# Performance work log

Hardware: AMD Instinct MI355X
Metric: run time of the kernel (lower is better)

The kernel has to match this reference:

```python
import jax, jax.numpy as jnp
import numpy as np

G = 8
NEIGHBORS = 9
EPS = 1e-5


def grid_sample_bilinear_border(img, grid):
    # img: [B, C, H, W], grid: [B, Hg, Wg, 2] with (x, y) in [-1, 1]
    # matches torch.nn.functional.grid_sample(mode='bilinear', padding_mode='border', align_corners=False)
    B, C, H, W = img.shape
    gx, gy = grid[..., 0], grid[..., 1]
    ix = jnp.clip(((gx + 1.0) * W - 1.0) * 0.5, 0.0, W - 1.0)
    iy = jnp.clip(((gy + 1.0) * H - 1.0) * 0.5, 0.0, H - 1.0)
    x0 = jnp.floor(ix); y0 = jnp.floor(iy)
    x1 = x0 + 1.0;      y1 = y0 + 1.0
    w00 = (x1 - ix) * (y1 - iy)
    w01 = (ix - x0) * (y1 - iy)
    w10 = (x1 - ix) * (iy - y0)
    w11 = (ix - x0) * (iy - y0)
    x0i = jnp.clip(x0, 0, W - 1).astype(jnp.int32)
    x1i = jnp.clip(x1, 0, W - 1).astype(jnp.int32)
    y0i = jnp.clip(y0, 0, H - 1).astype(jnp.int32)
    y1i = jnp.clip(y1, 0, H - 1).astype(jnp.int32)

    def gather(im, yy, xx):  # im [C,H,W], yy/xx [Hg,Wg] -> [C,Hg,Wg]
        return im[:, yy, xx]

    g = jax.vmap(gather)
    out = (g(img, y0i, x0i) * w00[:, None]
         + g(img, y0i, x1i) * w01[:, None]
         + g(img, y1i, x0i) * w10[:, None]
         + g(img, y1i, x1i) * w11[:, None])
    return out  # [B, C, Hg, Wg]


def pconv(x, w):
    # 1x1x1 conv3d (no bias): x [B,Cin,D,H,W], w [Cout,Cin]
    return jnp.einsum('bcdhw,oc->bodhw', x, w)


def bn_relu(x, gamma, beta):
    # BatchNorm3d (training-mode batch stats, biased variance) + ReLU
    mean = jnp.mean(x, axis=(0, 2, 3, 4), keepdims=True)
    var = jnp.var(x, axis=(0, 2, 3, 4), keepdims=True)
    xn = (x - mean) * jax.lax.rsqrt(var + EPS)
    return jax.nn.relu(xn * gamma.reshape(1, -1, 1, 1, 1) + beta.reshape(1, -1, 1, 1, 1))


def setup_inputs() -> dict:
    key = jax.random.key(0)
    ks = jax.random.split(key, 8)
    B, C, H, W = 2, 64, 256, 320
    ref_feature = jax.random.normal(ks[0], (B, C, H, W), dtype=jnp.float32)
    grid = jax.random.uniform(ks[1], (B, NEIGHBORS * H, W, 2), dtype=jnp.float32,
                              minval=-1.0, maxval=1.0)
    s0 = 1.0 / np.sqrt(G)
    w0 = jax.random.uniform(ks[2], (16, G), jnp.float32, -s0, s0)
    g0 = jnp.ones((16,), jnp.float32); b0 = jnp.zeros((16,), jnp.float32)
    s1 = 1.0 / np.sqrt(16)
    w1 = jax.random.uniform(ks[3], (8, 16), jnp.float32, -s1, s1)
    g1 = jnp.ones((8,), jnp.float32); b1 = jnp.zeros((8,), jnp.float32)
    s2 = 1.0 / np.sqrt(8)
    ws = jax.random.uniform(ks[4], (1, 8), jnp.float32, -s2, s2)
    bs = jax.random.uniform(ks[5], (1,), jnp.float32, -s2, s2)
    return {"ref_feature": ref_feature, "grid": grid,
            "w0": w0, "g0": g0, "b0": b0,
            "w1": w1, "g1": g1, "b1": b1,
            "ws": ws, "bs": bs}


def reference(ref_feature, grid, w0, g0, b0, w1, g1, b1, ws, bs):
    B, C, H, W = ref_feature.shape
    x = grid_sample_bilinear_border(ref_feature, grid)          # [B, C, 9H, W]
    ref = ref_feature.reshape(B, G, C // G, H, W)               # [B, G, C/G, H, W]
    x = x.reshape(B, G, C // G, NEIGHBORS, H, W)
    x = jnp.mean(x * ref[:, :, :, None], axis=2)                # [B, G, 9, H, W]
    x = bn_relu(pconv(x, w0), g0, b0)                           # [B, 16, 9, H, W]
    x = bn_relu(pconv(x, w1), g1, b1)                           # [B, 8, 9, H, W]
    s = pconv(x, ws) + bs.reshape(1, -1, 1, 1, 1)               # [B, 1, 9, H, W]
    return jax.nn.sigmoid(jnp.squeeze(s, axis=1))               # [B, 9, H, W]
```

## Files before the change

kernel.cpp:

```cpp
#include <hip/hip_runtime.h>
#include <math.h>


constexpr int   Bc  = 2;
constexpr int   Cc  = 64;
constexpr int   Hc  = 256;
constexpr int   Wc  = 320;
constexpr int   NBc = 9;
constexpr int   HWc = Hc * Wc;
constexpr int   NPIX = Bc * HWc;
constexpr int   NPT  = Bc * NBc * HWc;
constexpr float EPSV = 1e-5f;

constexpr int NBLK_S = NPIX / 32;
constexpr int NB1    = 1024;
constexpr int NB2    = 1024;

constexpr size_t OFF_FEATB = 0;
constexpr size_t OFF_SB    = OFF_FEATB + (size_t)NPIX * 32;
constexpr size_t OFF_YM    = OFF_SB + (size_t)NPT * 4;
constexpr size_t OFF_ZM    = OFF_YM + 32;

__device__ __forceinline__ unsigned short f2bf_rne(float v) {
  unsigned int u = __float_as_uint(v);
  unsigned int r = (u + 0x7fffu + ((u >> 16) & 1u)) >> 16;
  return (unsigned short)r;
}
__device__ __forceinline__ void unpack8(uint4 u, float f[8]) {
  f[0] = __uint_as_float(u.x << 16);
  f[1] = __uint_as_float(u.x & 0xffff0000u);
  f[2] = __uint_as_float(u.y << 16);
  f[3] = __uint_as_float(u.y & 0xffff0000u);
  f[4] = __uint_as_float(u.z << 16);
  f[5] = __uint_as_float(u.z & 0xffff0000u);
  f[6] = __uint_as_float(u.w << 16);
  f[7] = __uint_as_float(u.w & 0xffff0000u);
}

__global__ __launch_bounds__(256) void k_transpose(
    const float* __restrict__ feat, unsigned short* __restrict__ featB,
    float* __restrict__ ymom) {
  if (blockIdx.x == 0 && threadIdx.x < 48) ymom[threadIdx.x] = 0.f;
  __shared__ float lds[64][65];
  const int tid  = threadIdx.x;
  const int b    = blockIdx.x / (HWc / 64);
  const int tile = blockIdx.x % (HWc / 64);
  const int hw0  = tile * 64;
  const int p    = tid & 63;
  const int ty   = tid >> 6;

  const float* src = feat + (size_t)b * Cc * HWc + hw0 + p;
#pragma unroll
  for (int c0 = 0; c0 < 64; c0 += 4) {
    lds[c0 + ty][p] = src[(size_t)(c0 + ty) * HWc];
  }
  __syncthreads();
  const int ch = tid & 63;
  unsigned short* dst = featB + ((size_t)b * HWc + hw0) * 64 + ch;
#pragma unroll
  for (int p0 = 0; p0 < 64; p0 += 4) {
    dst[(size_t)(p0 + ty) * 64] = f2bf_rne(lds[ch][p0 + ty]);
  }
}

__global__ __launch_bounds__(256) void k_sample(
    const float* __restrict__ grid, const unsigned short* __restrict__ featB,
    unsigned short* __restrict__ sOut) {
  const int tid = threadIdx.x;
  const int cid = blockIdx.x * 32 + (tid >> 3);
  const int j   = tid & 7;
  const int b   = cid / HWc;
  const int hw  = cid - b * HWc;
  const int h   = hw / Wc;
  const int w   = hw - h * Wc;

  const uint4* fbAll = (const uint4*)featB;
  const uint4 ur = fbAll[(size_t)cid * 8 + j];
  float r[8];
  unpack8(ur, r);

  const uint4* fb = fbAll + (size_t)b * HWc * 8;

#pragma unroll 3
  for (int n = 0; n < NBc; ++n) {
    const size_t gi = ((((size_t)b * NBc + n) * Hc + h) * Wc + w) * 2;
    const float2 g2 = *(const float2*)(grid + gi);
    float ix = ((g2.x + 1.f) * (float)Wc - 1.f) * 0.5f;
    float iy = ((g2.y + 1.f) * (float)Hc - 1.f) * 0.5f;
    ix = fminf(fmaxf(ix, 0.f), (float)(Wc - 1));
    iy = fminf(fmaxf(iy, 0.f), (float)(Hc - 1));
    const float x0f = floorf(ix), y0f = floorf(iy);
    const float fx = ix - x0f, fy = iy - y0f;
    const int x0 = (int)x0f, y0 = (int)y0f;
    const int x1 = min(x0 + 1, Wc - 1), y1 = min(y0 + 1, Hc - 1);
    const float w00 = (1.f - fx) * (1.f - fy);
    const float w01 = fx * (1.f - fy);
    const float w10 = (1.f - fx) * fy;
    const float w11 = fx * fy;

    const uint4 u00 = fb[(size_t)(y0 * Wc + x0) * 8 + j];
    const uint4 u01 = fb[(size_t)(y0 * Wc + x1) * 8 + j];
    const uint4 u10 = fb[(size_t)(y1 * Wc + x0) * 8 + j];
    const uint4 u11 = fb[(size_t)(y1 * Wc + x1) * 8 + j];
    float a[8], c[8], d[8], e[8];
    unpack8(u00, a);
    unpack8(u01, c);
    unpack8(u10, d);
    unpack8(u11, e);

    float s = 0.f;
#pragma unroll
    for (int k = 0; k < 8; ++k) {
      s += (w00 * a[k] + w01 * c[k] + w10 * d[k] + w11 * e[k]) * r[k];
    }
    s *= 0.125f;

    const size_t pt = ((size_t)b * NBc + n) * HWc + hw;
    sOut[pt * 8 + j] = f2bf_rne(s);
  }
}

__global__ __launch_bounds__(256) void k_stats1(
    const unsigned short* __restrict__ sB, const float* __restrict__ w0,
    float* __restrict__ ymom) {
  __shared__ float w0s[128];
  __shared__ float red[4 * 32];
  const int tid = threadIdx.x;
  if (tid < 128) w0s[tid] = w0[tid];
  __syncthreads();

  float sy[16], sy2[16];
#pragma unroll
  for (int c = 0; c < 16; ++c) { sy[c] = 0.f; sy2[c] = 0.f; }

  const int stride = gridDim.x * blockDim.x;
  for (int p = blockIdx.x * blockDim.x + tid; p < NPT; p += stride) {
    const uint4 su = ((const uint4*)sB)[p];
    float s[8];
    unpack8(su, s);
#pragma unroll
    for (int c = 0; c < 16; ++c) {
      const float* wr = w0s + c * 8;
      float y = 0.f;
#pragma unroll
      for (int k = 0; k < 8; ++k) y += wr[k] * s[k];
      sy[c] += y;
      sy2[c] += y * y;
    }
  }
#pragma unroll
  for (int c = 0; c < 16; ++c) {
    for (int off = 32; off >= 1; off >>= 1) {
      sy[c] += __shfl_xor(sy[c], off);
      sy2[c] += __shfl_xor(sy2[c], off);
    }
  }
  const int wid = tid >> 6;
  if ((tid & 63) == 0) {
#pragma unroll
    for (int c = 0; c < 16; ++c) {
      red[wid * 32 + c] = sy[c];
      red[wid * 32 + 16 + c] = sy2[c];
    }
  }
  __syncthreads();
  if (tid < 32) {
    atomicAdd(&ymom[tid],
              red[tid] + red[32 + tid] + red[64 + tid] + red[96 + tid]);
  }
}

__global__ __launch_bounds__(256) void k_stats2(
    const unsigned short* __restrict__ sB, const float* __restrict__ ymom,
    const float* __restrict__ w0, const float* __restrict__ w1,
    const float* __restrict__ g0, const float* __restrict__ b0,
    float* __restrict__ zmom) {
  __shared__ float w0s[128], w1s[128], a1s[16], c1s[16];
  __shared__ float red[4 * 16];
  const int tid = threadIdx.x;
  if (tid < 128) { w0s[tid] = w0[tid]; w1s[tid] = w1[tid]; }
  if (tid < 16) {
    const float invN = 1.f / (float)NPT;
    const float mean = ymom[tid] * invN;
    const float var = ymom[16 + tid] * invN - mean * mean;
    const float a = g0[tid] * rsqrtf(var + EPSV);
    a1s[tid] = a;
    c1s[tid] = b0[tid] - mean * a;
  }
  __syncthreads();

  float sz[8], sz2[8];
#pragma unroll
  for (int o = 0; o < 8; ++o) { sz[o] = 0.f; sz2[o] = 0.f; }

  const int stride = gridDim.x * blockDim.x;
  for (int p = blockIdx.x * blockDim.x + tid; p < NPT; p += stride) {
    const uint4 su = ((const uint4*)sB)[p];
    float s[8];
    unpack8(su, s);
    float x1[16];
#pragma unroll
    for (int c = 0; c < 16; ++c) {
      const float* wr = w0s + c * 8;
      float y = 0.f;
#pragma unroll
      for (int k = 0; k < 8; ++k) y += wr[k] * s[k];
      x1[c] = fmaxf(a1s[c] * y + c1s[c], 0.f);
    }
#pragma unroll
    for (int o = 0; o < 8; ++o) {
      const float* wr = w1s + o * 16;
      float z = 0.f;
#pragma unroll
      for (int k = 0; k < 16; ++k) z += wr[k] * x1[k];
      sz[o] += z;
      sz2[o] += z * z;
    }
  }
#pragma unroll
  for (int o = 0; o < 8; ++o) {
    for (int off = 32; off >= 1; off >>= 1) {
      sz[o] += __shfl_xor(sz[o], off);
      sz2[o] += __shfl_xor(sz2[o], off);
    }
  }
  const int wid = tid >> 6;
  if ((tid & 63) == 0) {
#pragma unroll
    for (int o = 0; o < 8; ++o) {
      red[wid * 16 + o] = sz[o];
      red[wid * 16 + 8 + o] = sz2[o];
    }
  }
  __syncthreads();
  if (tid < 16) {
    atomicAdd(&zmom[tid],
              red[tid] + red[16 + tid] + red[32 + tid] + red[48 + tid]);
  }
}

__global__ __launch_bounds__(256) void k_final(
    const unsigned short* __restrict__ sB, const float* __restrict__ ymom,
    const float* __restrict__ zmom, const float* __restrict__ w0,
    const float* __restrict__ w1, const float* __restrict__ g0,
    const float* __restrict__ b0, const float* __restrict__ g1,
    const float* __restrict__ b1, const float* __restrict__ wsW,
    const float* __restrict__ bs, float* __restrict__ out) {
  __shared__ float w0s[128], w1s[128], a1s[16], c1s[16], a2s[8], c2s[8], wss[8];
  __shared__ float bss;
  const int tid = threadIdx.x;
  if (tid < 128) { w0s[tid] = w0[tid]; w1s[tid] = w1[tid]; }
  if (tid < 16) {
    const float invN = 1.f / (float)NPT;
    const float mean = ymom[tid] * invN;
    const float var = ymom[16 + tid] * invN - mean * mean;
    const float a = g0[tid] * rsqrtf(var + EPSV);
    a1s[tid] = a;
    c1s[tid] = b0[tid] - mean * a;
  }
  if (tid >= 128 && tid < 136) {
    const int o = tid - 128;
    const float invN = 1.f / (float)NPT;
    const float mean = zmom[o] * invN;
    const float var = zmom[8 + o] * invN - mean * mean;
    const float a = g1[o] * rsqrtf(var + EPSV);
    a2s[o] = a;
    c2s[o] = b1[o] - mean * a;
    wss[o] = wsW[o];
  }
  if (tid == 255) bss = bs[0];
  __syncthreads();

  const int p = blockIdx.x * blockDim.x + tid;
  if (p >= NPT) return;
  const uint4 su = ((const uint4*)sB)[p];
  float s[8];
  unpack8(su, s);
  float x1[16];
#pragma unroll
  for (int c = 0; c < 16; ++c) {
    const float* wr = w0s + c * 8;
    float y = 0.f;
#pragma unroll
    for (int k = 0; k < 8; ++k) y += wr[k] * s[k];
    x1[c] = fmaxf(a1s[c] * y + c1s[c], 0.f);
  }
  float o = bss;
#pragma unroll
  for (int oc = 0; oc < 8; ++oc) {
    const float* wr = w1s + oc * 16;
    float z = 0.f;
#pragma unroll
    for (int k = 0; k < 16; ++k) z += wr[k] * x1[k];
    const float x2 = fmaxf(a2s[oc] * z + c2s[oc], 0.f);
    o += wss[oc] * x2;
  }
  out[p] = 1.f / (1.f + expf(-o));
}

extern "C" void kernel_launch(void* const* d_in, const int* in_sizes, int n_in,
                              void* d_out, int out_size, void* d_ws,
                              size_t ws_size, hipStream_t stream) {
  const float* feat = (const float*)d_in[0];
  const float* grid = (const float*)d_in[1];
  const float* w0 = (const float*)d_in[2];
  const float* g0 = (const float*)d_in[3];
  const float* b0 = (const float*)d_in[4];
  const float* w1 = (const float*)d_in[5];
  const float* g1 = (const float*)d_in[6];
  const float* b1 = (const float*)d_in[7];
  const float* wsW = (const float*)d_in[8];
  const float* bs = (const float*)d_in[9];
  float* out = (float*)d_out;

  float* wsf = (float*)d_ws;
  unsigned short* featB = (unsigned short*)(wsf + OFF_FEATB);
  unsigned short* sB    = (unsigned short*)(wsf + OFF_SB);
  float* ymom = wsf + OFF_YM;
  float* zmom = wsf + OFF_ZM;

  k_transpose<<<Bc * (HWc / 64), 256, 0, stream>>>(feat, featB, ymom);
  k_sample<<<NBLK_S, 256, 0, stream>>>(grid, featB, sB);
  k_stats1<<<NB1, 256, 0, stream>>>(sB, w0, ymom);
  k_stats2<<<NB2, 256, 0, stream>>>(sB, ymom, w0, w1, g0, b0, zmom);
  k_final<<<(NPT + 255) / 256, 256, 0, stream>>>(sB, ymom, zmom, w0, w1, g0, b0,
                                                 g1, b1, wsW, bs, out);
}
```

Measured before the change: 258.7 us.

## Batch four points per thread and replace stat atomics with per-block partials

```diff
diff --git a/kernel.cpp b/kernel.cpp
--- a/kernel.cpp
+++ b/kernel.cpp
@@ -13,13 +13,15 @@
 constexpr float EPSV = 1e-5f;
 
 constexpr int NBLK_S = NPIX / 32;
-constexpr int NB1    = 1024;
-constexpr int NB2    = 1024;
+constexpr int NGRP   = NPT / 1024;
+constexpr int NB1    = 720;
+constexpr int NB2    = 720;
+constexpr int NBF    = 720;
 
 constexpr size_t OFF_FEATB = 0;
 constexpr size_t OFF_SB    = OFF_FEATB + (size_t)NPIX * 32;
-constexpr size_t OFF_YM    = OFF_SB + (size_t)NPT * 4;
-constexpr size_t OFF_ZM    = OFF_YM + 32;
+constexpr size_t OFF_P1    = 0;
+constexpr size_t OFF_P2    = OFF_P1 + (size_t)NB1 * 32;
 
 __device__ __forceinline__ unsigned short f2bf_rne(float v) {
   unsigned int u = __float_as_uint(v);
@@ -36,11 +38,13 @@
   f[6] = __uint_as_float(u.w << 16);
   f[7] = __uint_as_float(u.w & 0xffff0000u);
 }
+__device__ __forceinline__ float dot8(const float s[8], float4 wa, float4 wb) {
+  return s[0] * wa.x + s[1] * wa.y + s[2] * wa.z + s[3] * wa.w +
+         s[4] * wb.x + s[5] * wb.y + s[6] * wb.z + s[7] * wb.w;
+}
 
 __global__ __launch_bounds__(256) void k_transpose(
-    const float* __restrict__ feat, unsigned short* __restrict__ featB,
-    float* __restrict__ ymom) {
-  if (blockIdx.x == 0 && threadIdx.x < 48) ymom[threadIdx.x] = 0.f;
+    const float* __restrict__ feat, unsigned short* __restrict__ featB) {
   __shared__ float lds[64][65];
   const int tid  = threadIdx.x;
   const int b    = blockIdx.x / (HWc / 64);
@@ -122,7 +126,7 @@
 
 __global__ __launch_bounds__(256) void k_stats1(
     const unsigned short* __restrict__ sB, const float* __restrict__ w0,
-    float* __restrict__ ymom) {
+    float* __restrict__ part1) {
   __shared__ float w0s[128];
   __shared__ float red[4 * 32];
   const int tid = threadIdx.x;
@@ -133,19 +137,27 @@
 #pragma unroll
   for (int c = 0; c < 16; ++c) { sy[c] = 0.f; sy2[c] = 0.f; }
 
-  const int stride = gridDim.x * blockDim.x;
-  for (int p = blockIdx.x * blockDim.x + tid; p < NPT; p += stride) {
-    const uint4 su = ((const uint4*)sB)[p];
-    float s[8];
-    unpack8(su, s);
+  for (int g = blockIdx.x; g < NGRP; g += NB1) {
+    const uint4* src = (const uint4*)sB + (size_t)g * 1024 + tid;
+    float s[4][8];
+#pragma unroll
+    for (int i = 0; i < 4; ++i) {
+      const uint4 su = src[i * 256];
+      unpack8(su, s[i]);
+    }
 #pragma unroll
     for (int c = 0; c < 16; ++c) {
-      const float* wr = w0s + c * 8;
-      float y = 0.f;
-#pragma unroll
-      for (int k = 0; k < 8; ++k) y += wr[k] * s[k];
-      sy[c] += y;
-      sy2[c] += y * y;
+      const float4 wa = *(const float4*)(w0s + c * 8);
+      const float4 wb = *(const float4*)(w0s + c * 8 + 4);
+      float ay = 0.f, ay2 = 0.f;
+#pragma unroll
+      for (int i = 0; i < 4; ++i) {
+        const float y = dot8(s[i], wa, wb);
+        ay += y;
+        ay2 += y * y;
+      }
+      sy[c] += ay;
+      sy2[c] += ay2;
     }
   }
 #pragma unroll
@@ -165,24 +177,41 @@
   }
   __syncthreads();
   if (tid < 32) {
-    atomicAdd(&ymom[tid],
-              red[tid] + red[32 + tid] + red[64 + tid] + red[96 + tid]);
+    part1[blockIdx.x * 32 + tid] =
+        red[tid] + red[32 + tid] + red[64 + tid] + red[96 + tid];
   }
 }
 
 __global__ __launch_bounds__(256) void k_stats2(
-    const unsigned short* __restrict__ sB, const float* __restrict__ ymom,
+    const unsigned short* __restrict__ sB, const float* __restrict__ part1,
     const float* __restrict__ w0, const float* __restrict__ w1,
     const float* __restrict__ g0, const float* __restrict__ b0,
-    float* __restrict__ zmom) {
-  __shared__ float w0s[128], w1s[128], a1s[16], c1s[16];
-  __shared__ float red[4 * 16];
+    float* __restrict__ part2) {
+  __shared__ float w0s[128], w1ts[128], a1s[16], c1s[16];
+  __shared__ float red[256];
   const int tid = threadIdx.x;
-  if (tid < 128) { w0s[tid] = w0[tid]; w1s[tid] = w1[tid]; }
+  if (tid < 128) {
+    w0s[tid] = w0[tid];
+    w1ts[(tid & 15) * 8 + (tid >> 4)] = w1[tid];
+  }
+  {
+    const int c = tid & 31, chk = tid >> 5;
+    float acc = 0.f;
+    for (int r = chk; r < NB1; r += 8) acc += part1[r * 32 + c];
+    red[tid] = acc;
+  }
+  __syncthreads();
+  if (tid < 32) {
+    float v = 0.f;
+#pragma unroll
+    for (int k = 0; k < 8; ++k) v += red[k * 32 + tid];
+    red[tid] = v;
+  }
+  __syncthreads();
   if (tid < 16) {
     const float invN = 1.f / (float)NPT;
-    const float mean = ymom[tid] * invN;
-    const float var = ymom[16 + tid] * invN - mean * mean;
+    const float mean = red[tid] * invN;
+    const float var = red[16 + tid] * invN - mean * mean;
     const float a = g0[tid] * rsqrtf(var + EPSV);
     a1s[tid] = a;
     c1s[tid] = b0[tid] - mean * a;
@@ -193,29 +222,44 @@
 #pragma unroll
   for (int o = 0; o < 8; ++o) { sz[o] = 0.f; sz2[o] = 0.f; }
 
-  const int stride = gridDim.x * blockDim.x;
-  for (int p = blockIdx.x * blockDim.x + tid; p < NPT; p += stride) {
-    const uint4 su = ((const uint4*)sB)[p];
-    float s[8];
-    unpack8(su, s);
-    float x1[16];
+  for (int g = blockIdx.x; g < NGRP; g += NB2) {
+    const uint4* src = (const uint4*)sB + (size_t)g * 1024 + tid;
+    float s[4][8];
+#pragma unroll
+    for (int i = 0; i < 4; ++i) {
+      const uint4 su = src[i * 256];
+      unpack8(su, s[i]);
+    }
+    float z[4][8];
+#pragma unroll
+    for (int i = 0; i < 4; ++i)
+#pragma unroll
+      for (int o = 0; o < 8; ++o) z[i][o] = 0.f;
+
 #pragma unroll
     for (int c = 0; c < 16; ++c) {
-      const float* wr = w0s + c * 8;
-      float y = 0.f;
-#pragma unroll
-      for (int k = 0; k < 8; ++k) y += wr[k] * s[k];
-      x1[c] = fmaxf(a1s[c] * y + c1s[c], 0.f);
-    }
-#pragma unroll
-    for (int o = 0; o < 8; ++o) {
-      const float* wr = w1s + o * 16;
-      float z = 0.f;
-#pragma unroll
-      for (int k = 0; k < 16; ++k) z += wr[k] * x1[k];
-      sz[o] += z;
-      sz2[o] += z * z;
-    }
+      const float4 wa = *(const float4*)(w0s + c * 8);
+      const float4 wb = *(const float4*)(w0s + c * 8 + 4);
+      const float4 ta = *(const float4*)(w1ts + c * 8);
+      const float4 tb = *(const float4*)(w1ts + c * 8 + 4);
+      const float a1c = a1s[c], c1c = c1s[c];
+#pragma unroll
+      for (int i = 0; i < 4; ++i) {
+        const float y = dot8(s[i], wa, wb);
+        const float x = fmaxf(a1c * y + c1c, 0.f);
+        z[i][0] += ta.x * x; z[i][1] += ta.y * x;
+        z[i][2] += ta.z * x; z[i][3] += ta.w * x;
+        z[i][4] += tb.x * x; z[i][5] += tb.y * x;
+        z[i][6] += tb.z * x; z[i][7] += tb.w * x;
+      }
+    }
+#pragma unroll
+    for (int i = 0; i < 4; ++i)
+#pragma unroll
+      for (int o = 0; o < 8; ++o) {
+        sz[o] += z[i][o];
+        sz2[o] += z[i][o] * z[i][o];
+      }
   }
 #pragma unroll
   for (int o = 0; o < 8; ++o) {
@@ -234,68 +278,127 @@
   }
   __syncthreads();
   if (tid < 16) {
-    atomicAdd(&zmom[tid],
-              red[tid] + red[16 + tid] + red[32 + tid] + red[48 + tid]);
+    part2[blockIdx.x * 16 + tid] =
+        red[tid] + red[16 + tid] + red[32 + tid] + red[48 + tid];
   }
 }
 
 __global__ __launch_bounds__(256) void k_final(
-    const unsigned short* __restrict__ sB, const float* __restrict__ ymom,
-    const float* __restrict__ zmom, const float* __restrict__ w0,
+    const unsigned short* __restrict__ sB, const float* __restrict__ part1,
+    const float* __restrict__ part2, const float* __restrict__ w0,
     const float* __restrict__ w1, const float* __restrict__ g0,
     const float* __restrict__ b0, const float* __restrict__ g1,
     const float* __restrict__ b1, const float* __restrict__ wsW,
     const float* __restrict__ bs, float* __restrict__ out) {
-  __shared__ float w0s[128], w1s[128], a1s[16], c1s[16], a2s[8], c2s[8], wss[8];
+  __shared__ float w0s[128], w1ts[128], a1s[16], c1s[16], a2s[8], c2s[8],
+      wss[8];
   __shared__ float bss;
+  __shared__ float red[256];
   const int tid = threadIdx.x;
-  if (tid < 128) { w0s[tid] = w0[tid]; w1s[tid] = w1[tid]; }
+  if (tid < 128) {
+    w0s[tid] = w0[tid];
+    w1ts[(tid & 15) * 8 + (tid >> 4)] = w1[tid];
+  }
+  if (tid >= 128 && tid < 136) wss[tid - 128] = wsW[tid - 128];
+  if (tid == 136) bss = bs[0];
+  {
+    const int c = tid & 31, chk = tid >> 5;
+    float acc = 0.f;
+    for (int r = chk; r < NB1; r += 8) acc += part1[r * 32 + c];
+    red[tid] = acc;
+  }
+  __syncthreads();
+  if (tid < 32) {
+    float v = 0.f;
+#pragma unroll
+    for (int k = 0; k < 8; ++k) v += red[k * 32 + tid];
+    red[tid] = v;
+  }
+  __syncthreads();
   if (tid < 16) {
     const float invN = 1.f / (float)NPT;
-    const float mean = ymom[tid] * invN;
-    const float var = ymom[16 + tid] * invN - mean * mean;
+    const float mean = red[tid] * invN;
+    const float var = red[16 + tid] * invN - mean * mean;
     const float a = g0[tid] * rsqrtf(var + EPSV);
     a1s[tid] = a;
     c1s[tid] = b0[tid] - mean * a;
   }
-  if (tid >= 128 && tid < 136) {
-    const int o = tid - 128;
+  __syncthreads();
+  {
+    const int c = tid & 15, chk = tid >> 4;
+    float acc = 0.f;
+    for (int r = chk; r < NB2; r += 16) acc += part2[r * 16 + c];
+    red[tid] = acc;
+  }
+  __syncthreads();
+  if (tid < 16) {
+    float v = 0.f;
+#pragma unroll
+    for (int k = 0; k < 16; ++k) v += red[k * 16 + tid];
+    red[tid] = v;
+  }
+  __syncthreads();
+  if (tid < 8) {
     const float invN = 1.f / (float)NPT;
-    const float mean = zmom[o] * invN;
-    const float var = zmom[8 + o] * invN - mean * mean;
-    const float a = g1[o] * rsqrtf(var + EPSV);
-    a2s[o] = a;
-    c2s[o] = b1[o] - mean * a;
-    wss[o] = wsW[o];
-  }
-  if (tid == 255) bss = bs[0];
-  __syncthreads();
-
-  const int p = blockIdx.x * blockDim.x + tid;
-  if (p >= NPT) return;
-  const uint4 su = ((const uint4*)sB)[p];
-  float s[8];
-  unpack8(su, s);
-  float x1[16];
-#pragma unroll
-  for (int c = 0; c < 16; ++c) {
-    const float* wr = w0s + c * 8;
-    float y = 0.f;
-#pragma unroll
-    for (int k = 0; k < 8; ++k) y += wr[k] * s[k];
-    x1[c] = fmaxf(a1s[c] * y + c1s[c], 0.f);
-  }
-  float o = bss;
-#pragma unroll
-  for (int oc = 0; oc < 8; ++oc) {
-    const float* wr = w1s + oc * 16;
-    float z = 0.f;
-#pragma unroll
-    for (int k = 0; k < 16; ++k) z += wr[k] * x1[k];
-    const float x2 = fmaxf(a2s[oc] * z + c2s[oc], 0.f);
-    o += wss[oc] * x2;
-  }
-  out[p] = 1.f / (1.f + expf(-o));
+    const float mean = red[tid] * invN;
+    const float var = red[8 + tid] * invN - mean * mean;
+    const float a = g1[tid] * rsqrtf(var + EPSV);
+    a2s[tid] = a;
+    c2s[tid] = b1[tid] - mean * a;
+  }
+  __syncthreads();
+
+  float a2r[8], c2r[8], wsr[8];
+#pragma unroll
+  for (int o = 0; o < 8; ++o) {
+    a2r[o] = a2s[o];
+    c2r[o] = c2s[o];
+    wsr[o] = wss[o];
+  }
+  const float bsr = bss;
+
+  for (int g = blockIdx.x; g < NGRP; g += NBF) {
+    const uint4* src = (const uint4*)sB + (size_t)g * 1024 + tid;
+    float s[4][8];
+#pragma unroll
+    for (int i = 0; i < 4; ++i) {
+      const uint4 su = src[i * 256];
+      unpack8(su, s[i]);
+    }
+    float z[4][8];
+#pragma unroll
+    for (int i = 0; i < 4; ++i)
+#pragma unroll
+      for (int o = 0; o < 8; ++o) z[i][o] = 0.f;
+
+#pragma unroll
+    for (int c = 0; c < 16; ++c) {
+      const float4 wa = *(const float4*)(w0s + c * 8);
+      const float4 wb = *(const float4*)(w0s + c * 8 + 4);
+      const float4 ta = *(const float4*)(w1ts + c * 8);
+      const float4 tb = *(const float4*)(w1ts + c * 8 + 4);
+      const float a1c = a1s[c], c1c = c1s[c];
+#pragma unroll
+      for (int i = 0; i < 4; ++i) {
+        const float y = dot8(s[i], wa, wb);
+        const float x = fmaxf(a1c * y + c1c, 0.f);
+        z[i][0] += ta.x * x; z[i][1] += ta.y * x;
+        z[i][2] += ta.z * x; z[i][3] += ta.w * x;
+        z[i][4] += tb.x * x; z[i][5] += tb.y * x;
+        z[i][6] += tb.z * x; z[i][7] += tb.w * x;
+      }
+    }
+#pragma unroll
+    for (int i = 0; i < 4; ++i) {
+      float o = bsr;
+#pragma unroll
+      for (int oc = 0; oc < 8; ++oc) {
+        const float x2 = fmaxf(a2r[oc] * z[i][oc] + c2r[oc], 0.f);
+        o += wsr[oc] * x2;
+      }
+      out[(size_t)g * 1024 + i * 256 + tid] = 1.f / (1.f + expf(-o));
+    }
+  }
 }
 
 extern "C" void kernel_launch(void* const* d_in, const int* in_sizes, int n_in,
@@ -316,13 +419,13 @@
   float* wsf = (float*)d_ws;
   unsigned short* featB = (unsigned short*)(wsf + OFF_FEATB);
   unsigned short* sB    = (unsigned short*)(wsf + OFF_SB);
-  float* ymom = wsf + OFF_YM;
-  float* zmom = wsf + OFF_ZM;
-
-  k_transpose<<<Bc * (HWc / 64), 256, 0, stream>>>(feat, featB, ymom);
+  float* part1 = wsf + OFF_P1;
+  float* part2 = wsf + OFF_P2;
+
+  k_transpose<<<Bc * (HWc / 64), 256, 0, stream>>>(feat, featB);
   k_sample<<<NBLK_S, 256, 0, stream>>>(grid, featB, sB);
-  k_stats1<<<NB1, 256, 0, stream>>>(sB, w0, ymom);
-  k_stats2<<<NB2, 256, 0, stream>>>(sB, ymom, w0, w1, g0, b0, zmom);
-  k_final<<<(NPT + 255) / 256, 256, 0, stream>>>(sB, ymom, zmom, w0, w1, g0, b0,
-                                                 g1, b1, wsW, bs, out);
-}
+  k_stats1<<<NB1, 256, 0, stream>>>(sB, w0, part1);
+  k_stats2<<<NB2, 256, 0, stream>>>(sB, part1, w0, w1, g0, b0, part2);
+  k_final<<<NBF, 256, 0, stream>>>(sB, part1, part2, w0, w1, g0, b0, g1, b1,
+                                   wsW, bs, out);
+}
```

Result: slower. 483.8 us (+87.0%).
